# Performance work log

Measured on AMD Instinct MI355X. Metric: run time of the kernel, lower is better.

The kernel has to match this reference:

```python
import jax, jax.numpy as jnp
import numpy as np

GRID_SIZE = 5
SPLINE_ORDER = 3
N_COEF = GRID_SIZE + SPLINE_ORDER  # 8
NUM_NODES = 100000
NUM_EDGES = 1200000
NUM_GRAPHS = 512
D = 64
N_TARGETS = 10


def _grid():
    # uniform grid on [-1, 1] extended by spline_order knots on each side (efficient-kan default)
    h = 2.0 / GRID_SIZE
    return jnp.arange(-SPLINE_ORDER, GRID_SIZE + SPLINE_ORDER + 1, dtype=jnp.float32) * h - 1.0


def b_splines(x):
    # x: (N, in) -> (N, in, N_COEF) via Cox-de Boor recursion
    g = _grid()
    xe = x[..., None]
    bases = ((xe >= g[:-1]) & (xe < g[1:])).astype(x.dtype)
    for k in range(1, SPLINE_ORDER + 1):
        left = (xe - g[: -(k + 1)]) / (g[k:-1] - g[: -(k + 1)])
        right = (g[k + 1:] - xe) / (g[k + 1:] - g[1:-k])
        bases = left * bases[..., :-1] + right * bases[..., 1:]
    return bases


def kan_linear(x, base_w, spline_w, scaler):
    # efficient-kan KANLinear: silu base branch + standalone-scaled spline branch
    base = jax.nn.silu(x) @ base_w.T
    sb = b_splines(x)  # (N, in, N_COEF)
    spline = jnp.einsum('nig,oig->no', sb, spline_w * scaler[..., None])
    return base + spline


def setup_inputs() -> dict:
    key = jax.random.key(0)
    ks = jax.random.split(key, 12)
    inp = {
        'x': jax.random.normal(ks[0], (NUM_NODES, D), dtype=jnp.float32),
        'edge_index': jax.random.randint(ks[1], (2, NUM_EDGES), 0, NUM_NODES, dtype=jnp.int64),
        'batch': jnp.sort(jax.random.randint(ks[2], (NUM_NODES,), 0, NUM_GRAPHS, dtype=jnp.int64)),
        # GINConv layer 0 KAN (D -> D)
        'base_w0': jax.random.normal(ks[3], (D, D), dtype=jnp.float32) * 0.1,
        'spline_w0': jax.random.normal(ks[4], (D, D, N_COEF), dtype=jnp.float32) * 0.1,
        'scaler0': jax.random.normal(ks[5], (D, D), dtype=jnp.float32) * 0.1 + 1.0,
        # GINConv layer 1 KAN (D -> D)
        'base_w1': jax.random.normal(ks[6], (D, D), dtype=jnp.float32) * 0.1,
        'spline_w1': jax.random.normal(ks[7], (D, D, N_COEF), dtype=jnp.float32) * 0.1,
        'scaler1': jax.random.normal(ks[8], (D, D), dtype=jnp.float32) * 0.1 + 1.0,
        # head KAN (D -> N_TARGETS)
        'base_wh': jax.random.normal(ks[9], (N_TARGETS, D), dtype=jnp.float32) * 0.1,
        'spline_wh': jax.random.normal(ks[10], (N_TARGETS, D, N_COEF), dtype=jnp.float32) * 0.1,
        'scaler_h': jax.random.normal(ks[11], (N_TARGETS, D), dtype=jnp.float32) * 0.1 + 1.0,
    }
    return inp


def reference(x, edge_index, batch, base_w0, spline_w0, scaler0,
              base_w1, spline_w1, scaler1, base_wh, spline_wh, scaler_h):
    src, dst = edge_index[0], edge_index[1]
    n = x.shape[0]
    # GINConv layer 0: nn((1+eps)*x + sum_{j in N(i)} x_j), eps=0; dropout is eval-mode identity
    agg = jax.ops.segment_sum(x[src], dst, num_segments=n)
    h = kan_linear(x + agg, base_w0, spline_w0, scaler0)
    # GINConv layer 1
    agg = jax.ops.segment_sum(h[src], dst, num_segments=n)
    h = kan_linear(h + agg, base_w1, spline_w1, scaler1)
    # global_add_pool over graphs, then KAN head
    pooled = jax.ops.segment_sum(h, batch, num_segments=NUM_GRAPHS)
    return kan_linear(pooled, base_wh, spline_wh, scaler_h)
```

## Files before the change

### kernel.cpp

```cpp
#include <hip/hip_runtime.h>
#include <hip/hip_fp16.h>
#include <math.h>

#define NODES   100000
#define EDGES   1200000
#define GRAPHS  512
#define DIM     64
#define NT      10
#define KTOT    576

#define NB      512
#define NBUSED  391
#define EPB     4096
#define CAP     4608
#define COLBUF  2048

#define KSTAGE     96
#define WTL_STRIDE 104
#define V_STRIDE   72

#define PREP_BLOCKS 288

typedef _Float16 f16x8  __attribute__((ext_vector_type(8)));
typedef __fp16   fp16x2 __attribute__((ext_vector_type(2)));
typedef __attribute__((ext_vector_type(4))) float frag_cd;

__device__ __forceinline__ float silu(float x) {
    return x / (1.f + __expf(-x));
}

__device__ __forceinline__ unsigned packh2(float a, float b) {
    fp16x2 h = __builtin_amdgcn_cvt_pkrtz(a, b);
    return __builtin_bit_cast(unsigned, h);
}

__device__ __forceinline__ void acc_h8(float* a, uint4 p) {
    union { uint4 u; __half2 h[4]; } up; up.u = p;
#pragma unroll
    for (int j = 0; j < 4; ++j) {
        float2 f = __half22float2(up.h[j]);
        a[2 * j]     += f.x;
        a[2 * j + 1] += f.y;
    }
}

__device__ __forceinline__ f16x8 bases_frag(float xv) {
    float tt  = fmaf(xv, 2.5f, 5.5f);
    float fm  = floorf(tt);
    int   m   = (int)fm;
    float u   = tt - fm;
    float um1 = 1.f - u;
    float v3  = u * u * u * (1.f / 6.f);
    float v0  = um1 * um1 * um1 * (1.f / 6.f);
    float B2m1 = 0.5f * ((u + 1.f) * um1 + (2.f - u) * u);
    float v1  = ((u + 2.f) * um1 * um1 * 0.5f + (2.f - u) * B2m1) * (1.f / 3.f);
    float v2  = ((u + 1.f) * B2m1 + (3.f - u) * u * u * 0.5f) * (1.f / 3.f);

    unsigned d0 = packh2(v0, v1);
    unsigned d1 = packh2(v2, v3);
    int p = m - 3;
    int B = p >> 1;
    bool odd = (p & 1) != 0;
    unsigned e1 = __builtin_amdgcn_alignbit(d1, d0, 16);
    unsigned W0 = odd ? (d0 << 16) : d0;
    unsigned W1 = odd ? e1 : d1;
    unsigned W2 = odd ? (d1 >> 16) : 0u;
    union { f16x8 f; unsigned u[4]; } r;
    r.u[0] = (B == 0) ? W0 : ((B == -1) ? W1 : ((B == -2) ? W2 : 0u));
    r.u[1] = (B == 1) ? W0 : ((B ==  0) ? W1 : ((B == -1) ? W2 : 0u));
    r.u[2] = (B == 2) ? W0 : ((B ==  1) ? W1 : ((B ==  0) ? W2 : 0u));
    r.u[3] = (B == 3) ? W0 : ((B ==  2) ? W1 : ((B ==  1) ? W2 : 0u));
    return r.f;
}

__global__ void prep_conv(const float* __restrict__ bw0, const float* __restrict__ sw0,
                          const float* __restrict__ sc0,
                          const float* __restrict__ bw1, const float* __restrict__ sw1,
                          const float* __restrict__ sc1,
                          unsigned short* __restrict__ wt0,
                          unsigned short* __restrict__ wt1,
                          const float* __restrict__ x, const int* __restrict__ bat,
                          unsigned short* __restrict__ xb,
                          unsigned short* __restrict__ hpad,
                          int* __restrict__ goff) {
    int bx = blockIdx.x;
    if (bx < PREP_BLOCKS) {
        int idx = bx * 256 + threadIdx.x;
        int layer = idx >= DIM * KTOT;
        int li = layer ? idx - DIM * KTOT : idx;
        const float* bw = layer ? bw1 : bw0;
        const float* sw = layer ? sw1 : sw0;
        const float* sc = layer ? sc1 : sc0;
        unsigned short* wt = layer ? wt1 : wt0;
        int o = li / KTOT, k = li % KTOT;
        float v;
        if (k < DIM) {
            v = bw[o * DIM + k];
        } else {
            int i = (k - DIM) >> 3, g = (k - DIM) & 7;
            v = sw[(o * DIM + i) * 8 + g] * sc[o * DIM + i];
        }
        wt[li] = __half_as_ushort(__float2half(v));
        return;
    }
    int i = (bx - PREP_BLOCKS) * 256 + threadIdx.x;
    if (i < NODES * 16) {
        float4 v = ((const float4*)x)[i];
        unsigned lo = packh2(v.x, v.y);
        unsigned hi = packh2(v.z, v.w);
        ((uint2*)xb)[i] = make_uint2(lo, hi);
        if ((i & 15) == 0) {
            int n = i >> 4;
            int b  = bat[n];
            int bp = (n == 0) ? -1 : bat[n - 1];
            for (int g = bp + 1; g <= b; ++g) goff[g] = n;
        }
        if (i == 0) {
            int blast = bat[NODES - 1];
            for (int g = blast + 1; g <= GRAPHS; ++g) goff[g] = NODES;
        }
    } else {
        int j = i - NODES * 16;
        if (j < 16)      ((uint2*)xb)[NODES * 16 + j] = make_uint2(0, 0);
        else if (j < 32) ((uint2*)hpad)[j - 16]       = make_uint2(0, 0);
    }
}

__global__ __launch_bounds__(256) void s3_partition(const int* __restrict__ ei,
                                                    int* __restrict__ bcur,
                                                    unsigned* __restrict__ tmp) {
    __shared__ int hist[NB], gbase[NB], cur[NB];
    int t = threadIdx.x;
    hist[t] = 0; hist[t + 256] = 0;
    cur[t]  = 0; cur[t + 256]  = 0;
    __syncthreads();
    int e0 = blockIdx.x * EPB;
    int src[16], dst[16];
#pragma unroll
    for (int k = 0; k < 16; ++k) {
        int e = e0 + t + k * 256;
        bool valid = e < EDGES;
        src[k] = valid ? ei[e] : 0;
        dst[k] = valid ? ei[EDGES + e] : -1;
        if (valid) atomicAdd(&hist[dst[k] >> 8], 1);
    }
    __syncthreads();
    {
        int c0 = hist[t];       if (c0) gbase[t]       = atomicAdd(&bcur[t], c0);
        int c1 = hist[t + 256]; if (c1) gbase[t + 256] = atomicAdd(&bcur[t + 256], c1);
    }
    __syncthreads();
#pragma unroll
    for (int k = 0; k < 16; ++k) {
        if (dst[k] >= 0) {
            int b = dst[k] >> 8;
            int slot = atomicAdd(&cur[b], 1);
            tmp[(size_t)b * CAP + gbase[b] + slot] =
                (unsigned)src[k] | ((unsigned)(dst[k] & 255) << 24);
        }
    }
}

__global__ __launch_bounds__(256) void s4_fill(const unsigned* __restrict__ tmp,
                                               const int* __restrict__ bcur,
                                               int2* __restrict__ rowp,
                                               int* __restrict__ col) {
    __shared__ int hist[256], scan[256], tot;
    __shared__ int4 colbuf4[CAP / 4];
    int* colbuf = (int*)colbuf4;
    int b = blockIdx.x, t = threadIdx.x;
    int cnt = bcur[b];
    int base = b * CAP;
    hist[t] = 0;
    __syncthreads();
    for (int i = t; i < cnt; i += 256)
        atomicAdd(&hist[tmp[base + i] >> 24], 1);
    __syncthreads();
    int deg = hist[t];
    int pad = (deg + 3) & ~3;
    scan[t] = pad;
    __syncthreads();
    int run = pad;
    for (int d = 1; d < 256; d <<= 1) {
        int a = (t >= d) ? scan[t - d] : 0;
        __syncthreads();
        run += a; scan[t] = run;
        __syncthreads();
    }
    int start = run - pad;
    int ng = b * 256 + t;
    if (ng < NODES) rowp[ng] = make_int2(base + start, base + start + pad);
    if (t == 255) tot = run;
    __syncthreads();
    scan[t] = start;
    __syncthreads();
    for (int i = t; i < cnt; i += 256) {
        unsigned p = tmp[base + i];
        int pos = atomicAdd(&scan[p >> 24], 1);
        colbuf[pos] = (int)(p & 0xFFFFFFu);
    }
    __syncthreads();
    for (int k = scan[t]; k < start + pad; ++k) colbuf[k] = NODES;
    __syncthreads();
    int nq = tot >> 2;
    int4* out4 = (int4*)(col + base);
    for (int i = t; i < nq; i += 256) out4[i] = colbuf4[i];
}

__global__ __launch_bounds__(256) void fused_layer(const unsigned short* __restrict__ xin,
                                                   const int2* __restrict__ rowp,
                                                   const int* __restrict__ col,
                                                   const unsigned short* __restrict__ wt,
                                                   unsigned short* __restrict__ out) {
    __shared__ unsigned short wt_lds[64 * WTL_STRIDE];
    __shared__ unsigned short v_lds[64 * V_STRIDE];
    __shared__ int4 col4_lds[COLBUF / 4];
    __shared__ int cinfo[2];

    const int t     = threadIdx.x;
    const int nbase = blockIdx.x * 64;

    uint4 p0, p1, p2;
    {
        int c0 = t, c1 = t + 256, c2 = t + 512;
        p0 = *(const uint4*)(wt + (c0 / 12) * KTOT + (c0 % 12) * 8);
        p1 = *(const uint4*)(wt + (c1 / 12) * KTOT + (c1 % 12) * 8);
        p2 = *(const uint4*)(wt + (c2 / 12) * KTOT + (c2 % 12) * 8);
    }

    if (t == 0) {
        int cbeg = rowp[nbase].x;
        int last = nbase + 63 < NODES ? nbase + 63 : NODES - 1;
        int cend = rowp[last].y;
        cinfo[0] = cbeg;
        cinfo[1] = cend - cbeg;
    }
    __syncthreads();
    const int cbeg = cinfo[0];
    const int span = cinfo[1];
    const bool lds_cols = (span <= COLBUF);
    if (lds_cols) {
        const int4* g4 = (const int4*)(col + cbeg);
        for (int i = t; i < (span >> 2); i += 256) col4_lds[i] = g4[i];
    }
    __syncthreads();

    const uint4* x4 = (const uint4*)xin;
#pragma unroll
    for (int rd = 0; rd < 2; ++rd) {
        int idx  = t + rd * 256;
        int node = idx >> 3, c8 = idx & 7;
        int n = nbase + node;
        uint4 res = make_uint4(0, 0, 0, 0);
        if (n < NODES) {
            int2 be = rowp[n];
            float a0[8], a1[8], a2[8], a3[8];
#pragma unroll
            for (int j = 0; j < 8; ++j) { a0[j] = 0.f; a1[j] = 0.f; a2[j] = 0.f; a3[j] = 0.f; }
            acc_h8(a0, x4[n * 8 + c8]);
            if (lds_cols) {
                for (int p = be.x; p < be.y; p += 4) {
                    int4 c4 = *(const int4*)((const int*)col4_lds + (p - cbeg));
                    uint4 r0 = x4[c4.x * 8 + c8];
                    uint4 r1 = x4[c4.y * 8 + c8];
                    uint4 r2 = x4[c4.z * 8 + c8];
                    uint4 r3 = x4[c4.w * 8 + c8];
                    acc_h8(a0, r0); acc_h8(a1, r1); acc_h8(a2, r2); acc_h8(a3, r3);
                }
            } else {
                for (int p = be.x; p < be.y; p += 4) {
                    int4 c4 = *(const int4*)(col + p);
                    uint4 r0 = x4[c4.x * 8 + c8];
                    uint4 r1 = x4[c4.y * 8 + c8];
                    uint4 r2 = x4[c4.z * 8 + c8];
                    uint4 r3 = x4[c4.w * 8 + c8];
                    acc_h8(a0, r0); acc_h8(a1, r1); acc_h8(a2, r2); acc_h8(a3, r3);
                }
            }
            union { uint4 u; unsigned w[4]; } rr;
#pragma unroll
            for (int j = 0; j < 4; ++j) {
                float lo = a0[2 * j]     + a1[2 * j]     + a2[2 * j]     + a3[2 * j];
                float hi = a0[2 * j + 1] + a1[2 * j + 1] + a2[2 * j + 1] + a3[2 * j + 1];
                rr.w[j] = packh2(lo, hi);
            }
            res = rr.u;
        }
        *(uint4*)(v_lds + node * V_STRIDE + c8 * 8) = res;
    }
    {
        int c0 = t, c1 = t + 256, c2 = t + 512;
        *(uint4*)(wt_lds + (c0 / 12) * WTL_STRIDE + (c0 % 12) * 8) = p0;
        *(uint4*)(wt_lds + (c1 / 12) * WTL_STRIDE + (c1 % 12) * 8) = p1;
        *(uint4*)(wt_lds + (c2 / 12) * WTL_STRIDE + (c2 % 12) * 8) = p2;
    }
    __syncthreads();

    const int w = t >> 6;
    const int l = t & 63;
    const int q = l >> 4;
    const int c = l & 15;
    const unsigned short* vrow = v_lds + ((w << 4) + c) * V_STRIDE;

    frag_cd ac0 = {0.f, 0.f, 0.f, 0.f};
    frag_cd ac1 = {0.f, 0.f, 0.f, 0.f};
    frag_cd ac2 = {0.f, 0.f, 0.f, 0.f};
    frag_cd ac3 = {0.f, 0.f, 0.f, 0.f};

#define MSTEP(OFF, A) {                                                          \
        f16x8 b0 = *(const f16x8*)(wt_lds + (c     ) * WTL_STRIDE + (OFF));      \
        f16x8 b1 = *(const f16x8*)(wt_lds + (c + 16) * WTL_STRIDE + (OFF));      \
        f16x8 b2 = *(const f16x8*)(wt_lds + (c + 32) * WTL_STRIDE + (OFF));      \
        f16x8 b3 = *(const f16x8*)(wt_lds + (c + 48) * WTL_STRIDE + (OFF));      \
        ac0 = __builtin_amdgcn_mfma_f32_16x16x32_f16(A, b0, ac0, 0, 0, 0);       \
        ac1 = __builtin_amdgcn_mfma_f32_16x16x32_f16(A, b1, ac1, 0, 0, 0);       \
        ac2 = __builtin_amdgcn_mfma_f32_16x16x32_f16(A, b2, ac2, 0, 0, 0);       \
        ac3 = __builtin_amdgcn_mfma_f32_16x16x32_f16(A, b3, ac3, 0, 0, 0); }

    {
        int c0 = t, c1 = t + 256, c2 = t + 512;
        p0 = *(const uint4*)(wt + (c0 / 12) * KTOT + KSTAGE + (c0 % 12) * 8);
        p1 = *(const uint4*)(wt + (c1 / 12) * KTOT + KSTAGE + (c1 % 12) * 8);
        p2 = *(const uint4*)(wt + (c2 / 12) * KTOT + KSTAGE + (c2 % 12) * 8);
    }

#pragma unroll
    for (int s = 0; s < 2; ++s) {
        f16x8 hv = *(const f16x8*)(vrow + 32 * s + 8 * q);
        float f[8];
#pragma unroll
        for (int j = 0; j < 8; ++j) f[j] = silu((float)hv[j]);
        union { f16x8 v; unsigned u[4]; } a;
#pragma unroll
        for (int j = 0; j < 4; ++j) a.u[j] = packh2(f[2 * j], f[2 * j + 1]);
        MSTEP(32 * s + 8 * q, a.v);
    }
    {
        f16x8 a = bases_frag((float)(*(const _Float16*)(vrow + q)));
        MSTEP(64 + 8 * q, a);
    }

#pragma unroll
    for (int st = 1; st < 6; ++st) {
        __syncthreads();
        {
            int c0 = t, c1 = t + 256, c2 = t + 512;
            *(uint4*)(wt_lds + (c0 / 12) * WTL_STRIDE + (c0 % 12) * 8) = p0;
            *(uint4*)(wt_lds + (c1 / 12) * WTL_STRIDE + (c1 % 12) * 8) = p1;
            *(uint4*)(wt_lds + (c2 / 12) * WTL_STRIDE + (c2 % 12) * 8) = p2;
        }
        __syncthreads();
        if (st < 5) {
            int c0 = t, c1 = t + 256, c2 = t + 512;
            p0 = *(const uint4*)(wt + (c0 / 12) * KTOT + (st + 1) * KSTAGE + (c0 % 12) * 8);
            p1 = *(const uint4*)(wt + (c1 / 12) * KTOT + (st + 1) * KSTAGE + (c1 % 12) * 8);
            p2 = *(const uint4*)(wt + (c2 / 12) * KTOT + (st + 1) * KSTAGE + (c2 % 12) * 8);
        }
#pragma unroll
        for (int k = 0; k < 3; ++k) {
            int s = 3 * st + k;
            f16x8 a = bases_frag((float)(*(const _Float16*)(vrow + 4 * s + q - 8)));
            MSTEP(32 * k + 8 * q, a);
        }
    }
#undef MSTEP

    const int n0 = nbase + (w << 4) + (q << 2);
#pragma unroll
    for (int r = 0; r < 4; ++r) {
        int n = n0 + r;
        if (n < NODES) {
            unsigned short* o = out + (size_t)n * DIM + c;
            o[0]  = __half_as_ushort(__float2half(ac0[r]));
            o[16] = __half_as_ushort(__float2half(ac1[r]));
            o[32] = __half_as_ushort(__float2half(ac2[r]));
            o[48] = __half_as_ushort(__float2half(ac3[r]));
        }
    }
}

__global__ __launch_bounds__(256) void pool_head(const unsigned short* __restrict__ h,
                                                 const int* __restrict__ goff,
                                                 const float* __restrict__ bwh,
                                                 const float* __restrict__ swh,
                                                 const float* __restrict__ sch,
                                                 float* __restrict__ out) {
    __shared__ float ps[8][64];
    const int g = blockIdx.x, t = threadIdx.x;
    const int start = goff[g], end = goff[g + 1];
    const int d2 = t & 31, grp = t >> 5;
    float s0 = 0.f, s1 = 0.f;
    for (int n = start + grp; n < end; n += 8) {
        __half2 hv = *(const __half2*)(h + (size_t)n * DIM + 2 * d2);
        float2 f = __half22float2(hv);
        s0 += f.x;
        s1 += f.y;
    }
    ps[grp][2 * d2]     = s0;
    ps[grp][2 * d2 + 1] = s1;
    __syncthreads();

    if (t < 64) {
        const int i = t;
        float xv = 0.f;
#pragma unroll
        for (int k = 0; k < 8; ++k) xv += ps[k][i];

        float s  = silu(xv);
        float tt  = fmaf(xv, 2.5f, 5.5f);
        float fm  = floorf(tt);
        int   m   = (int)fm;
        float u   = tt - fm;
        float um1 = 1.f - u;
        float v3  = u * u * u * (1.f / 6.f);
        float v0  = um1 * um1 * um1 * (1.f / 6.f);
        float B2m1 = 0.5f * ((u + 1.f) * um1 + (2.f - u) * u);
        float v1  = ((u + 2.f) * um1 * um1 * 0.5f + (2.f - u) * B2m1) * (1.f / 3.f);
        float v2  = ((u + 1.f) * B2m1 + (3.f - u) * u * u * 0.5f) * (1.f / 3.f);
        bool inr  = (m >= 0) && (m <= 10);
        float b[8];
#pragma unroll
        for (int j = 0; j < 8; ++j) {
            float bv = 0.f;
            bv = (j == m - 3) ? v0 : bv;
            bv = (j == m - 2) ? v1 : bv;
            bv = (j == m - 1) ? v2 : bv;
            bv = (j == m)     ? v3 : bv;
            b[j] = inr ? bv : 0.f;
        }

        float part[NT];
#pragma unroll
        for (int o = 0; o < NT; ++o) {
            const float* sp = swh + (o * DIM + i) * 8;
            float sb = 0.f;
#pragma unroll
            for (int qq = 0; qq < 8; ++qq) sb = fmaf(b[qq], sp[qq], sb);
            part[o] = fmaf(s, bwh[o * DIM + i], sb * sch[o * DIM + i]);
        }
#pragma unroll
        for (int o = 0; o < NT; ++o) {
            float v = part[o];
#pragma unroll
            for (int off = 32; off > 0; off >>= 1) v += __shfl_down(v, off, 64);
            if (i == 0) out[g * NT + o] = v;
        }
    }
}

extern "C" void kernel_launch(void* const* d_in, const int* in_sizes, int n_in,
                              void* d_out, int out_size, void* d_ws, size_t ws_size,
                              hipStream_t stream) {
    const float* x   = (const float*)d_in[0];
    const int*   ei  = (const int*)d_in[1];
    const int*   bat = (const int*)d_in[2];
    const float* bw0 = (const float*)d_in[3];
    const float* sw0 = (const float*)d_in[4];
    const float* sc0 = (const float*)d_in[5];
    const float* bw1 = (const float*)d_in[6];
    const float* sw1 = (const float*)d_in[7];
    const float* sc1 = (const float*)d_in[8];
    const float* bwh = (const float*)d_in[9];
    const float* swh = (const float*)d_in[10];
    const float* sch = (const float*)d_in[11];
    float* out = (float*)d_out;

    const size_t ROW = (size_t)(NODES + 1) * DIM;

    unsigned short* wt0 = (unsigned short*)d_ws;
    unsigned short* wt1 = wt0 + DIM * KTOT;
    unsigned short* xbf = wt1 + DIM * KTOT;
    unsigned short* hbf = xbf + ROW;
    unsigned short* h2  = hbf + ROW;
    int* goff     = (int*)(h2 + (size_t)NODES * DIM);
    int2* rowp    = (int2*)(goff + 514);
    int* col      = (int*)(rowp + NODES);
    int* bcur     = col + (size_t)NB * CAP;
    unsigned* tmp = (unsigned*)(bcur + NB);

    const int conv_blocks = (NODES * 16 + 32 + 255) / 256;
    prep_conv<<<PREP_BLOCKS + conv_blocks, 256, 0, stream>>>(
        bw0, sw0, sc0, bw1, sw1, sc1, wt0, wt1,
        x, bat, xbf, hbf + (size_t)NODES * DIM, goff);

    (void)hipMemsetAsync(bcur, 0, NB * sizeof(int), stream);
    const int part_blocks = (EDGES + EPB - 1) / EPB;
    s3_partition<<<part_blocks, 256, 0, stream>>>(ei, bcur, tmp);
    s4_fill<<<NBUSED, 256, 0, stream>>>(tmp, bcur, rowp, col);

    const int layer_blocks = (NODES + 63) / 64;
    fused_layer<<<layer_blocks, 256, 0, stream>>>(xbf, rowp, col, wt0, hbf);
    fused_layer<<<layer_blocks, 256, 0, stream>>>(hbf, rowp, col, wt1, h2);

    pool_head<<<GRAPHS, 256, 0, stream>>>(h2, goff, bwh, swh, sch, out);
}
```

Before: 224.7 us.

## Merge edge partition with prep kernel and stage edges in LDS before scatter

Merges the edge-partition pass into the weight/feature prep launch as one 512-thread kernel, removing a launch and letting the independent work run concurrently. Inside the partition blocks, edges are now bucket-sorted in LDS with a prefix scan and then written out contiguously, aiming for more coalesced global stores. The fill kernel moves to 1024 threads. The fused layer drops its LDS staging of column indices and reads them straight from global memory, which saves a sync and LDS space but adds global traffic.

```diff
diff --git a/kernel.cpp b/kernel.cpp
--- a/kernel.cpp
+++ b/kernel.cpp
@@ -13,13 +13,14 @@
 #define NBUSED  391
 #define EPB     4096
 #define CAP     4608
-#define COLBUF  2048
 
 #define KSTAGE     96
 #define WTL_STRIDE 104
 #define V_STRIDE   72
 
-#define PREP_BLOCKS 288
+#define S3B     ((EDGES + EPB - 1) / EPB)
+#define PREPB   ((2 * DIM * KTOT) / 512)
+#define CONVB   ((NODES * 16 + 32 + 511) / 512)
 
 typedef _Float16 f16x8  __attribute__((ext_vector_type(8)));
 typedef __fp16   fp16x2 __attribute__((ext_vector_type(2)));
@@ -73,19 +74,75 @@
     return r.f;
 }
 
-__global__ void prep_conv(const float* __restrict__ bw0, const float* __restrict__ sw0,
-                          const float* __restrict__ sc0,
-                          const float* __restrict__ bw1, const float* __restrict__ sw1,
-                          const float* __restrict__ sc1,
-                          unsigned short* __restrict__ wt0,
-                          unsigned short* __restrict__ wt1,
-                          const float* __restrict__ x, const int* __restrict__ bat,
-                          unsigned short* __restrict__ xb,
-                          unsigned short* __restrict__ hpad,
-                          int* __restrict__ goff) {
-    int bx = blockIdx.x;
-    if (bx < PREP_BLOCKS) {
-        int idx = bx * 256 + threadIdx.x;
+__global__ __launch_bounds__(512) void mega(const int* __restrict__ ei,
+                                            int* __restrict__ bcur,
+                                            unsigned* __restrict__ tmp,
+                                            const float* __restrict__ bw0,
+                                            const float* __restrict__ sw0,
+                                            const float* __restrict__ sc0,
+                                            const float* __restrict__ bw1,
+                                            const float* __restrict__ sw1,
+                                            const float* __restrict__ sc1,
+                                            unsigned short* __restrict__ wt0,
+                                            unsigned short* __restrict__ wt1,
+                                            const float* __restrict__ x,
+                                            const int* __restrict__ bat,
+                                            unsigned short* __restrict__ xb,
+                                            unsigned short* __restrict__ hpad,
+                                            int* __restrict__ goff) {
+    __shared__ int hist[NB], lstart[NB], gbase[NB], cur[NB];
+    __shared__ unsigned ebuf[EPB];
+    __shared__ unsigned short bk[EPB];
+    const int bx = blockIdx.x;
+    const int t  = threadIdx.x;
+
+    if (bx < S3B) {
+        hist[t] = 0; cur[t] = 0;
+        __syncthreads();
+        const int e0 = bx * EPB;
+        int src[8], dst[8];
+#pragma unroll
+        for (int k = 0; k < 8; ++k) {
+            int e = e0 + t + k * 512;
+            bool valid = e < EDGES;
+            src[k] = valid ? ei[e] : 0;
+            dst[k] = valid ? ei[EDGES + e] : -1;
+            if (valid) atomicAdd(&hist[dst[k] >> 8], 1);
+        }
+        __syncthreads();
+        int v = hist[t];
+        lstart[t] = v;
+        __syncthreads();
+        int run = v;
+        for (int d = 1; d < NB; d <<= 1) {
+            int a = (t >= d) ? lstart[t - d] : 0;
+            __syncthreads();
+            run += a; lstart[t] = run;
+            __syncthreads();
+        }
+        lstart[t] = run - v;
+        if (v) gbase[t] = atomicAdd(&bcur[t], v);
+        __syncthreads();
+#pragma unroll
+        for (int k = 0; k < 8; ++k) {
+            if (dst[k] >= 0) {
+                int b = dst[k] >> 8;
+                int pos = lstart[b] + atomicAdd(&cur[b], 1);
+                ebuf[pos] = (unsigned)src[k] | ((unsigned)(dst[k] & 255) << 24);
+                bk[pos] = (unsigned short)b;
+            }
+        }
+        __syncthreads();
+        int total = EDGES - e0; if (total > EPB) total = EPB;
+        for (int i = t; i < total; i += 512) {
+            int b = bk[i];
+            tmp[(size_t)b * CAP + gbase[b] + (i - lstart[b])] = ebuf[i];
+        }
+        return;
+    }
+
+    if (bx < S3B + PREPB) {
+        int idx = (bx - S3B) * 512 + t;
         int layer = idx >= DIM * KTOT;
         int li = layer ? idx - DIM * KTOT : idx;
         const float* bw = layer ? bw1 : bw0;
@@ -103,7 +160,8 @@
         wt[li] = __half_as_ushort(__float2half(v));
         return;
     }
-    int i = (bx - PREP_BLOCKS) * 256 + threadIdx.x;
+
+    int i = (bx - S3B - PREPB) * 512 + t;
     if (i < NODES * 16) {
         float4 v = ((const float4*)x)[i];
         unsigned lo = packh2(v.x, v.y);
@@ -126,85 +184,55 @@
     }
 }
 
-__global__ __launch_bounds__(256) void s3_partition(const int* __restrict__ ei,
-                                                    int* __restrict__ bcur,
-                                                    unsigned* __restrict__ tmp) {
-    __shared__ int hist[NB], gbase[NB], cur[NB];
-    int t = threadIdx.x;
-    hist[t] = 0; hist[t + 256] = 0;
-    cur[t]  = 0; cur[t + 256]  = 0;
-    __syncthreads();
-    int e0 = blockIdx.x * EPB;
-    int src[16], dst[16];
-#pragma unroll
-    for (int k = 0; k < 16; ++k) {
-        int e = e0 + t + k * 256;
-        bool valid = e < EDGES;
-        src[k] = valid ? ei[e] : 0;
-        dst[k] = valid ? ei[EDGES + e] : -1;
-        if (valid) atomicAdd(&hist[dst[k] >> 8], 1);
-    }
-    __syncthreads();
-    {
-        int c0 = hist[t];       if (c0) gbase[t]       = atomicAdd(&bcur[t], c0);
-        int c1 = hist[t + 256]; if (c1) gbase[t + 256] = atomicAdd(&bcur[t + 256], c1);
-    }
-    __syncthreads();
-#pragma unroll
-    for (int k = 0; k < 16; ++k) {
-        if (dst[k] >= 0) {
-            int b = dst[k] >> 8;
-            int slot = atomicAdd(&cur[b], 1);
-            tmp[(size_t)b * CAP + gbase[b] + slot] =
-                (unsigned)src[k] | ((unsigned)(dst[k] & 255) << 24);
-        }
-    }
-}
-
-__global__ __launch_bounds__(256) void s4_fill(const unsigned* __restrict__ tmp,
-                                               const int* __restrict__ bcur,
-                                               int2* __restrict__ rowp,
-                                               int* __restrict__ col) {
-    __shared__ int hist[256], scan[256], tot;
+__global__ __launch_bounds__(1024) void s4_fill(const unsigned* __restrict__ tmp,
+                                                const int* __restrict__ bcur,
+                                                int2* __restrict__ rowp,
+                                                int* __restrict__ col) {
+    __shared__ int deg[256], scanI[256], cur[256];
+    __shared__ int tot;
     __shared__ int4 colbuf4[CAP / 4];
     int* colbuf = (int*)colbuf4;
-    int b = blockIdx.x, t = threadIdx.x;
-    int cnt = bcur[b];
-    int base = b * CAP;
-    hist[t] = 0;
-    __syncthreads();
-    for (int i = t; i < cnt; i += 256)
-        atomicAdd(&hist[tmp[base + i] >> 24], 1);
-    __syncthreads();
-    int deg = hist[t];
-    int pad = (deg + 3) & ~3;
-    scan[t] = pad;
-    __syncthreads();
-    int run = pad;
+    const int b = blockIdx.x, t = threadIdx.x;
+    const int cnt = bcur[b];
+    const int base = b * CAP;
+    if (t < 256) deg[t] = 0;
+    __syncthreads();
+    for (int i = t; i < cnt; i += 1024)
+        atomicAdd(&deg[tmp[base + i] >> 24], 1);
+    __syncthreads();
+    if (t < 256) scanI[t] = (deg[t] + 3) & ~3;
+    __syncthreads();
     for (int d = 1; d < 256; d <<= 1) {
-        int a = (t >= d) ? scan[t - d] : 0;
-        __syncthreads();
-        run += a; scan[t] = run;
-        __syncthreads();
-    }
-    int start = run - pad;
-    int ng = b * 256 + t;
-    if (ng < NODES) rowp[ng] = make_int2(base + start, base + start + pad);
-    if (t == 255) tot = run;
-    __syncthreads();
-    scan[t] = start;
-    __syncthreads();
-    for (int i = t; i < cnt; i += 256) {
+        int a = 0;
+        if (t < 256 && t >= d) a = scanI[t - d];
+        __syncthreads();
+        if (t < 256) scanI[t] += a;
+        __syncthreads();
+    }
+    if (t < 256) {
+        int pad = (deg[t] + 3) & ~3;
+        int start = scanI[t] - pad;
+        int ng = b * 256 + t;
+        if (ng < NODES) rowp[ng] = make_int2(base + start, base + start + pad);
+        cur[t] = start;
+        if (t == 255) tot = scanI[255];
+    }
+    __syncthreads();
+    for (int i = t; i < cnt; i += 1024) {
         unsigned p = tmp[base + i];
-        int pos = atomicAdd(&scan[p >> 24], 1);
+        int pos = atomicAdd(&cur[p >> 24], 1);
         colbuf[pos] = (int)(p & 0xFFFFFFu);
     }
     __syncthreads();
-    for (int k = scan[t]; k < start + pad; ++k) colbuf[k] = NODES;
+    if (t < 256) {
+        int pad = (deg[t] + 3) & ~3;
+        int end = scanI[t] - pad + pad;
+        for (int k = cur[t]; k < end; ++k) colbuf[k] = NODES;
+    }
     __syncthreads();
     int nq = tot >> 2;
     int4* out4 = (int4*)(col + base);
-    for (int i = t; i < nq; i += 256) out4[i] = colbuf4[i];
+    for (int i = t; i < nq; i += 1024) out4[i] = colbuf4[i];
 }
 
 __global__ __launch_bounds__(256) void fused_layer(const unsigned short* __restrict__ xin,
@@ -214,8 +242,6 @@
                                                    unsigned short* __restrict__ out) {
     __shared__ unsigned short wt_lds[64 * WTL_STRIDE];
     __shared__ unsigned short v_lds[64 * V_STRIDE];
-    __shared__ int4 col4_lds[COLBUF / 4];
-    __shared__ int cinfo[2];
 
     const int t     = threadIdx.x;
     const int nbase = blockIdx.x * 64;
@@ -227,23 +253,6 @@
         p1 = *(const uint4*)(wt + (c1 / 12) * KTOT + (c1 % 12) * 8);
         p2 = *(const uint4*)(wt + (c2 / 12) * KTOT + (c2 % 12) * 8);
     }
-
-    if (t == 0) {
-        int cbeg = rowp[nbase].x;
-        int last = nbase + 63 < NODES ? nbase + 63 : NODES - 1;
-        int cend = rowp[last].y;
-        cinfo[0] = cbeg;
-        cinfo[1] = cend - cbeg;
-    }
-    __syncthreads();
-    const int cbeg = cinfo[0];
-    const int span = cinfo[1];
-    const bool lds_cols = (span <= COLBUF);
-    if (lds_cols) {
-        const int4* g4 = (const int4*)(col + cbeg);
-        for (int i = t; i < (span >> 2); i += 256) col4_lds[i] = g4[i];
-    }
-    __syncthreads();
 
     const uint4* x4 = (const uint4*)xin;
 #pragma unroll
@@ -258,24 +267,13 @@
 #pragma unroll
             for (int j = 0; j < 8; ++j) { a0[j] = 0.f; a1[j] = 0.f; a2[j] = 0.f; a3[j] = 0.f; }
             acc_h8(a0, x4[n * 8 + c8]);
-            if (lds_cols) {
-                for (int p = be.x; p < be.y; p += 4) {
-                    int4 c4 = *(const int4*)((const int*)col4_lds + (p - cbeg));
-                    uint4 r0 = x4[c4.x * 8 + c8];
-                    uint4 r1 = x4[c4.y * 8 + c8];
-                    uint4 r2 = x4[c4.z * 8 + c8];
-                    uint4 r3 = x4[c4.w * 8 + c8];
-                    acc_h8(a0, r0); acc_h8(a1, r1); acc_h8(a2, r2); acc_h8(a3, r3);
-                }
-            } else {
-                for (int p = be.x; p < be.y; p += 4) {
-                    int4 c4 = *(const int4*)(col + p);
-                    uint4 r0 = x4[c4.x * 8 + c8];
-                    uint4 r1 = x4[c4.y * 8 + c8];
-                    uint4 r2 = x4[c4.z * 8 + c8];
-                    uint4 r3 = x4[c4.w * 8 + c8];
-                    acc_h8(a0, r0); acc_h8(a1, r1); acc_h8(a2, r2); acc_h8(a3, r3);
-                }
+            for (int p = be.x; p < be.y; p += 4) {
+                int4 c4 = *(const int4*)(col + p);
+                uint4 r0 = x4[c4.x * 8 + c8];
+                uint4 r1 = x4[c4.y * 8 + c8];
+                uint4 r2 = x4[c4.z * 8 + c8];
+                uint4 r3 = x4[c4.w * 8 + c8];
+                acc_h8(a0, r0); acc_h8(a1, r1); acc_h8(a2, r2); acc_h8(a3, r3);
             }
             union { uint4 u; unsigned w[4]; } rr;
 #pragma unroll
@@ -478,15 +476,14 @@
     int* bcur     = col + (size_t)NB * CAP;
     unsigned* tmp = (unsigned*)(bcur + NB);
 
-    const int conv_blocks = (NODES * 16 + 32 + 255) / 256;
-    prep_conv<<<PREP_BLOCKS + conv_blocks, 256, 0, stream>>>(
+    (void)hipMemsetAsync(bcur, 0, NB * sizeof(int), stream);
+
+    mega<<<S3B + PREPB + CONVB, 512, 0, stream>>>(
+        ei, bcur, tmp,
         bw0, sw0, sc0, bw1, sw1, sc1, wt0, wt1,
         x, bat, xbf, hbf + (size_t)NODES * DIM, goff);
 
-    (void)hipMemsetAsync(bcur, 0, NB * sizeof(int), stream);
-    const int part_blocks = (EDGES + EPB - 1) / EPB;
-    s3_partition<<<part_blocks, 256, 0, stream>>>(ei, bcur, tmp);
-    s4_fill<<<NBUSED, 256, 0, stream>>>(tmp, bcur, rowp, col);
+    s4_fill<<<NBUSED, 1024, 0, stream>>>(tmp, bcur, rowp, col);
 
     const int layer_blocks = (NODES + 63) / 64;
     fused_layer<<<layer_blocks, 256, 0, stream>>>(xbf, rowp, col, wt0, hbf);
```

New measurement: 214.3 us. -4.6%, faster.
